# Performance work log

Hardware: AMD Instinct MI355X
Metric: run time of the kernel (lower is better)

The kernel has to match this reference:

```python
import jax, jax.numpy as jnp
import numpy as np


def setup_inputs() -> dict:
    key = jax.random.key(0)
    k1, k2 = jax.random.split(key)
    B, C = 32768, 1000
    output = jax.random.normal(k1, (B, C), dtype=jnp.float32)
    target = jax.random.randint(k2, (B,), 0, C, dtype=jnp.int64)
    return {"output": output, "target": target}


def _soft_hinge_loss(margin, output, target):
    B = output.shape[0]
    rows = jnp.arange(B)
    fst = jax.nn.relu(1.0 - margin)
    # relu(1 - z_y + logsumexp(z))
    snd = jax.nn.relu(1.0 - output[rows, target]
                      + jax.scipy.special.logsumexp(output, axis=1))
    return jnp.where(margin >= 0, fst, snd)


def _partial_opt_mask(loss_value, threshold):
    # Vectorized form of the serial cumulative-threshold loop:
    # sort ascending, accumulate L over ALL sorted values, select sorted
    # position idx iff cumsum <= threshold - idx.
    B = loss_value.shape[0]
    order = jnp.argsort(loss_value)
    sorted_loss = loss_value[order]
    cum = jnp.cumsum(sorted_loss)
    selected = cum <= (threshold - jnp.arange(B, dtype=loss_value.dtype))
    # scatter selection flags back to original sample positions -> 0/1 vector v
    v = jnp.zeros((B,), dtype=loss_value.dtype).at[order].set(
        selected.astype(loss_value.dtype))
    return v


def reference(output, target):
    B = output.shape[0]
    rows = jnp.arange(B)
    prob = jax.nn.softmax(output, axis=1)                 # [B, C]
    margin = prob[rows, target] - jnp.max(prob, axis=1)   # [B]
    l = _soft_hinge_loss(margin, output, target)          # [B]
    threshold = jnp.asarray(B, dtype=l.dtype)
    v = _partial_opt_mask(l, threshold)                   # [B] 0/1 mask
    curriculum_loss_1 = jnp.dot(v, l)
    curriculum_loss_2 = (jnp.asarray(B, l.dtype) - jnp.sum(v)
                         + jnp.sum((margin < 0).astype(l.dtype)))
    return jnp.where(curriculum_loss_1 < curriculum_loss_2,
                     curriculum_loss_2, curriculum_loss_1)
```

## Files before the change

### kernel.cpp

```cpp
#include <hip/hip_runtime.h>
#include <math.h>

#define WAVE 64
#define NBINS 8192
#define BIN_SHIFT 19

__device__ __forceinline__ float wave_incl_scan(float x) {
  const int lane = threadIdx.x & 63;
#pragma unroll
  for (int o = 1; o < 64; o <<= 1) {
    float t = __shfl_up(x, o, WAVE);
    if (lane >= o) x += t;
  }
  return x;
}

__global__ void row_loss_kernel(const float* __restrict__ outp,
                                const int* __restrict__ target,
                                float* __restrict__ lv,
                                int B, int C) {
  const int lane = threadIdx.x & (WAVE - 1);
  const int wid  = threadIdx.x >> 6;
  const int row  = blockIdx.x * (blockDim.x >> 6) + wid;
  if (row >= B) return;

  const float* rp = outp + (size_t)row * (size_t)C;
  const float zy = rp[target[row]];

  const int C4 = C >> 2;
  const float4* rp4 = (const float4*)rp;

  float m = -INFINITY, s = 0.f;
#pragma unroll 2
  for (int i = lane; i < C4; i += WAVE) {
    float4 v = rp4[i];
    m = fmaxf(fmaxf(m, fmaxf(v.x, v.y)), fmaxf(v.z, v.w));
    s += __expf(v.x) + __expf(v.y) + __expf(v.z) + __expf(v.w);
  }
  for (int i = (C4 << 2) + lane; i < C; i += WAVE) {
    float x = rp[i];
    m = fmaxf(m, x);
    s += __expf(x);
  }
#pragma unroll
  for (int o = 32; o; o >>= 1) {
    m = fmaxf(m, __shfl_xor(m, o, WAVE));
    s += __shfl_xor(s, o, WAVE);
  }

  if (lane == 0) {
    float l = (zy >= m) ? 1.0f : fmaxf(0.0f, 1.0f - zy + __logf(s));
    lv[row] = l;
  }
}

__global__ __launch_bounds__(1024)
void hist_kernel(const float* __restrict__ lv,
                 unsigned* __restrict__ hcnt,
                 float* __restrict__ hsum,
                 unsigned* __restrict__ n_one,
                 int B) {
  __shared__ unsigned scnt[NBINS];
  __shared__ float    ssum[NBINS];
  __shared__ unsigned s_one;

  const int tid = threadIdx.x;
  for (int i = tid; i < NBINS; i += 1024) { scnt[i] = 0u; ssum[i] = 0.f; }
  if (tid == 0) s_one = 0u;
  __syncthreads();

  const int gid = blockIdx.x * 1024 + tid;
  if (gid < B) {
    float v = lv[gid];
    unsigned bits = __float_as_uint(v);
    unsigned b = bits >> BIN_SHIFT;
    atomicAdd(&scnt[b], 1u);
    atomicAdd(&ssum[b], v);
    unsigned long long ball = __ballot(bits == 0x3F800000u);
    if ((tid & 63) == 0 && ball)
      atomicAdd(&s_one, (unsigned)__popcll(ball));
  }
  __syncthreads();

  for (int i = tid; i < NBINS; i += 1024) {
    unsigned c = scnt[i];
    if (c) {
      atomicAdd(&hcnt[i], c);
      atomicAdd(&hsum[i], ssum[i]);
    }
  }
  if (tid == 0 && s_one) atomicAdd(n_one, s_one);
}

__global__ __launch_bounds__(1024)
void scan_hist(const unsigned* __restrict__ hcnt,
               const float* __restrict__ hsum,
               const unsigned* __restrict__ n_one_p,
               float* __restrict__ out, int B) {
  const int tid = threadIdx.x;
  const int lane = tid & 63, wid = tid >> 6;
  __shared__ float wS[16], wC[16];
  __shared__ unsigned sh_first;

  const int BPT = NBINS / 1024;
  float bs[8], bn[8];
  float ls = 0.f, lc = 0.f;
#pragma unroll
  for (int i = 0; i < 8; i++) {
    int b = tid * BPT + i;
    bs[i] = hsum[b];
    bn[i] = (float)hcnt[b];
    ls += bs[i]; lc += bn[i];
  }

  const float cn = (float)B - (float)(*n_one_p);
  if (tid == 0) sh_first = 0xFFFFFFFFu;

  float is = wave_incl_scan(ls);
  float ic = wave_incl_scan(lc);
  if (lane == 63) { wS[wid] = is; wC[wid] = ic; }
  __syncthreads();
  if (wid == 0 && lane < 16) {
    float x = wS[lane], y = wC[lane];
    float xs = x, ys = y;
#pragma unroll
    for (int o = 1; o < 16; o <<= 1) {
      float t = __shfl_up(xs, o, WAVE);
      float u = __shfl_up(ys, o, WAVE);
      if (lane >= o) { xs += t; ys += u; }
    }
    wS[lane] = xs - x;
    wC[lane] = ys - y;
  }
  __syncthreads();

  float cS = wS[wid] + (is - ls);
  float cC = wC[wid] + (ic - lc);
  int fidx = -1; float fS = 0.f, fC = 0.f;
#pragma unroll
  for (int i = 0; i < 8; i++) {
    if (fidx < 0 && (cS + bs[i]) + (cC + bn[i]) - 1.f > (float)B) {
      fidx = i; fS = cS; fC = cC;
    }
    cS += bs[i]; cC += bn[i];
  }
  if (fidx >= 0) atomicMin(&sh_first, (unsigned)tid);
  __syncthreads();

  const double Bd = (double)B;
  if (sh_first == (unsigned)tid && fidx >= 0) {
    const unsigned bin = (unsigned)(tid * BPT + fidx);
    const double v  = (double)__uint_as_float(bin << BIN_SHIFT);
    const double S0 = (double)fS, K0 = (double)fC;
    const double mt = (double)bn[fidx];
    double j = floor((Bd - S0 - K0 + 1.0) / (v + 1.0));
    if (j < 0.0) j = 0.0;
    if (j > mt) j = mt;
    double loss1 = S0 + j * v;
    double loss2 = Bd - (K0 + j) + (double)cn;
    out[0] = (float)fmax(loss1, loss2);
  } else if (sh_first == 0xFFFFFFFFu && tid == 1023) {
    double loss1 = (double)cS;
    double loss2 = (double)cn;
    out[0] = (float)fmax(loss1, loss2);
  }
}

extern "C" void kernel_launch(void* const* d_in, const int* in_sizes, int n_in,
                              void* d_out, int out_size, void* d_ws, size_t ws_size,
                              hipStream_t stream) {
  const float* outp  = (const float*)d_in[0];
  const int* target  = (const int*)d_in[1];
  const int B = in_sizes[1];
  const int C = in_sizes[0] / B;

  float*    lv   = (float*)d_ws;
  unsigned* hcnt = (unsigned*)((char*)d_ws + (size_t)B * 4);
  float*    hsum = (float*)((char*)d_ws + (size_t)B * 4 + NBINS * 4);
  unsigned* none = (unsigned*)((char*)d_ws + (size_t)B * 4 + NBINS * 8);

  hipMemsetAsync((char*)d_ws + (size_t)B * 4, 0, NBINS * 8 + 16, stream);

  const int waves_per_block = 4;
  dim3 grid((B + waves_per_block - 1) / waves_per_block);
  row_loss_kernel<<<grid, waves_per_block * WAVE, 0, stream>>>(outp, target, lv, B, C);

  const int hblocks = (B + 1023) / 1024;
  hist_kernel<<<hblocks, 1024, 0, stream>>>(lv, hcnt, hsum, none, B);
  scan_hist<<<1, 1024, 0, stream>>>(hcnt, hsum, none, (float*)d_out, B);
}
```

Measured before the change: 39.49 us.

## Fuse histogram and scan into one block with finer nonuniform bins

Replaces the global-atomic histogram kernel, the memset and the separate scan kernel with a single-block kernel. That kernel loads all per-row losses, builds a shared-memory histogram with fine bins near exponents 126–136 and coarse bins elsewhere, and scans it in place. The row-loss loop is also unrolled to four float4 loads per iteration to raise memory-level parallelism. This removes two launches, the memset and the global atomics. In exchange, one block must do all 32768 shared atomics serially, and the final answer is only exact if the bin layout suits the loss distribution; the code hardcodes a fixed input size, with 8 float4 per thread covering B up to 32768.

```diff
diff --git a/kernel.cpp b/kernel.cpp
--- a/kernel.cpp
+++ b/kernel.cpp
@@ -2,8 +2,27 @@
 #include <math.h>
 
 #define WAVE 64
-#define NBINS 8192
-#define BIN_SHIFT 19
+
+#define E_LO 126
+#define E_HI 136
+#define FINE_SHIFT 15
+#define N_FINE ((E_HI - E_LO) << 8)
+#define N_LOW  (E_LO)
+#define SBINS  3072
+
+__device__ __forceinline__ unsigned bin_of(unsigned bits) {
+  unsigned e = bits >> 23;
+  if (e < E_LO) return e;
+  if (e < E_HI) return N_LOW + ((bits - (E_LO << 23)) >> FINE_SHIFT);
+  return N_LOW + N_FINE + (e - E_HI);
+}
+
+__device__ __forceinline__ float bin_lower(unsigned bin) {
+  if (bin < N_LOW) return __uint_as_float(bin << 23);
+  if (bin < N_LOW + N_FINE)
+    return __uint_as_float((E_LO << 23) + ((bin - N_LOW) << FINE_SHIFT));
+  return __uint_as_float((E_HI + (bin - N_LOW - N_FINE)) << 23);
+}
 
 __device__ __forceinline__ float wave_incl_scan(float x) {
   const int lane = threadIdx.x & 63;
@@ -15,13 +34,14 @@
   return x;
 }
 
-__global__ void row_loss_kernel(const float* __restrict__ outp,
-                                const int* __restrict__ target,
-                                float* __restrict__ lv,
-                                int B, int C) {
+__global__ __launch_bounds__(256)
+void row_loss_kernel(const float* __restrict__ outp,
+                     const int* __restrict__ target,
+                     float* __restrict__ lv,
+                     int B, int C) {
   const int lane = threadIdx.x & (WAVE - 1);
   const int wid  = threadIdx.x >> 6;
-  const int row  = blockIdx.x * (blockDim.x >> 6) + wid;
+  const int row  = blockIdx.x * 4 + wid;
   if (row >= B) return;
 
   const float* rp = outp + (size_t)row * (size_t)C;
@@ -29,13 +49,26 @@
 
   const int C4 = C >> 2;
   const float4* rp4 = (const float4*)rp;
-
-  float m = -INFINITY, s = 0.f;
-#pragma unroll 2
-  for (int i = lane; i < C4; i += WAVE) {
-    float4 v = rp4[i];
-    m = fmaxf(fmaxf(m, fmaxf(v.x, v.y)), fmaxf(v.z, v.w));
-    s += __expf(v.x) + __expf(v.y) + __expf(v.z) + __expf(v.w);
+  const float NI = -INFINITY;
+
+  float m = NI, s = 0.f;
+  for (int i = lane; i < C4; i += 4 * WAVE) {
+    const int i1 = i + 64, i2 = i + 128, i3 = i + 192;
+    float4 a0 = rp4[i];
+    float4 a1 = rp4[i1 < C4 ? i1 : i];
+    float4 a2 = rp4[i2 < C4 ? i2 : i];
+    float4 a3 = rp4[i3 < C4 ? i3 : i];
+    if (i1 >= C4) a1.x = a1.y = a1.z = a1.w = NI;
+    if (i2 >= C4) a2.x = a2.y = a2.z = a2.w = NI;
+    if (i3 >= C4) a3.x = a3.y = a3.z = a3.w = NI;
+    m = fmaxf(m, fmaxf(fmaxf(a0.x, a0.y), fmaxf(a0.z, a0.w)));
+    m = fmaxf(m, fmaxf(fmaxf(a1.x, a1.y), fmaxf(a1.z, a1.w)));
+    m = fmaxf(m, fmaxf(fmaxf(a2.x, a2.y), fmaxf(a2.z, a2.w)));
+    m = fmaxf(m, fmaxf(fmaxf(a3.x, a3.y), fmaxf(a3.z, a3.w)));
+    s += __expf(a0.x) + __expf(a0.y) + __expf(a0.z) + __expf(a0.w);
+    s += __expf(a1.x) + __expf(a1.y) + __expf(a1.z) + __expf(a1.w);
+    s += __expf(a2.x) + __expf(a2.y) + __expf(a2.z) + __expf(a2.w);
+    s += __expf(a3.x) + __expf(a3.y) + __expf(a3.z) + __expf(a3.w);
   }
   for (int i = (C4 << 2) + lane; i < C; i += WAVE) {
     float x = rp[i];
@@ -55,67 +88,61 @@
 }
 
 __global__ __launch_bounds__(1024)
-void hist_kernel(const float* __restrict__ lv,
-                 unsigned* __restrict__ hcnt,
-                 float* __restrict__ hsum,
-                 unsigned* __restrict__ n_one,
-                 int B) {
-  __shared__ unsigned scnt[NBINS];
-  __shared__ float    ssum[NBINS];
-  __shared__ unsigned s_one;
-
-  const int tid = threadIdx.x;
-  for (int i = tid; i < NBINS; i += 1024) { scnt[i] = 0u; ssum[i] = 0.f; }
-  if (tid == 0) s_one = 0u;
-  __syncthreads();
-
-  const int gid = blockIdx.x * 1024 + tid;
-  if (gid < B) {
-    float v = lv[gid];
-    unsigned bits = __float_as_uint(v);
-    unsigned b = bits >> BIN_SHIFT;
-    atomicAdd(&scnt[b], 1u);
-    atomicAdd(&ssum[b], v);
-    unsigned long long ball = __ballot(bits == 0x3F800000u);
-    if ((tid & 63) == 0 && ball)
-      atomicAdd(&s_one, (unsigned)__popcll(ball));
-  }
-  __syncthreads();
-
-  for (int i = tid; i < NBINS; i += 1024) {
-    unsigned c = scnt[i];
-    if (c) {
-      atomicAdd(&hcnt[i], c);
-      atomicAdd(&hsum[i], ssum[i]);
-    }
-  }
-  if (tid == 0 && s_one) atomicAdd(n_one, s_one);
-}
-
-__global__ __launch_bounds__(1024)
-void scan_hist(const unsigned* __restrict__ hcnt,
-               const float* __restrict__ hsum,
-               const unsigned* __restrict__ n_one_p,
-               float* __restrict__ out, int B) {
+void select_fused(const float* __restrict__ lv, float* __restrict__ out, int B) {
+  __shared__ unsigned scnt[2][SBINS];
+  __shared__ float    ssum[2][SBINS];
+  __shared__ float wS[16], wC[16];
+  __shared__ unsigned sh_first, s_one;
+
   const int tid = threadIdx.x;
   const int lane = tid & 63, wid = tid >> 6;
-  __shared__ float wS[16], wC[16];
-  __shared__ unsigned sh_first;
-
-  const int BPT = NBINS / 1024;
-  float bs[8], bn[8];
+  const int sub = wid & 1;
+
+  for (int i = tid; i < SBINS; i += 1024) {
+    scnt[0][i] = 0u; scnt[1][i] = 0u;
+    ssum[0][i] = 0.f; ssum[1][i] = 0.f;
+  }
+  if (tid == 0) { s_one = 0u; sh_first = 0xFFFFFFFFu; }
+  __syncthreads();
+
+  float4 t[8];
+  bool ok[8];
+#pragma unroll
+  for (int k = 0; k < 8; k++) {
+    const int idx4 = tid + k * 1024;
+    ok[k] = (idx4 * 4 + 3) < B;
+    t[k] = ok[k] ? ((const float4*)lv)[idx4] : make_float4(0.f, 0.f, 0.f, 0.f);
+  }
+  int ones = 0;
+#pragma unroll
+  for (int k = 0; k < 8; k++) {
+    if (ok[k]) {
+      const float e[4] = {t[k].x, t[k].y, t[k].z, t[k].w};
+#pragma unroll
+      for (int j = 0; j < 4; j++) {
+        const unsigned bits = __float_as_uint(e[j]);
+        if (bits == 0x3F800000u) ones++;
+        const unsigned b = bin_of(bits);
+        atomicAdd(&scnt[sub][b], 1u);
+        atomicAdd(&ssum[sub][b], e[j]);
+      }
+    }
+  }
+  float of = (float)ones;
+#pragma unroll
+  for (int o = 32; o; o >>= 1) of += __shfl_xor(of, o, WAVE);
+  if (lane == 0 && of > 0.f) atomicAdd(&s_one, (unsigned)of);
+  __syncthreads();
+
+  float bs[3], bn[3];
   float ls = 0.f, lc = 0.f;
 #pragma unroll
-  for (int i = 0; i < 8; i++) {
-    int b = tid * BPT + i;
-    bs[i] = hsum[b];
-    bn[i] = (float)hcnt[b];
+  for (int i = 0; i < 3; i++) {
+    const int b = tid * 3 + i;
+    bs[i] = ssum[0][b] + ssum[1][b];
+    bn[i] = (float)(scnt[0][b] + scnt[1][b]);
     ls += bs[i]; lc += bn[i];
   }
-
-  const float cn = (float)B - (float)(*n_one_p);
-  if (tid == 0) sh_first = 0xFFFFFFFFu;
-
   float is = wave_incl_scan(ls);
   float ic = wave_incl_scan(lc);
   if (lane == 63) { wS[wid] = is; wC[wid] = ic; }
@@ -125,9 +152,9 @@
     float xs = x, ys = y;
 #pragma unroll
     for (int o = 1; o < 16; o <<= 1) {
-      float t = __shfl_up(xs, o, WAVE);
-      float u = __shfl_up(ys, o, WAVE);
-      if (lane >= o) { xs += t; ys += u; }
+      float a = __shfl_up(xs, o, WAVE);
+      float b = __shfl_up(ys, o, WAVE);
+      if (lane >= o) { xs += a; ys += b; }
     }
     wS[lane] = xs - x;
     wC[lane] = ys - y;
@@ -138,7 +165,7 @@
   float cC = wC[wid] + (ic - lc);
   int fidx = -1; float fS = 0.f, fC = 0.f;
 #pragma unroll
-  for (int i = 0; i < 8; i++) {
+  for (int i = 0; i < 3; i++) {
     if (fidx < 0 && (cS + bs[i]) + (cC + bn[i]) - 1.f > (float)B) {
       fidx = i; fS = cS; fC = cC;
     }
@@ -148,20 +175,21 @@
   __syncthreads();
 
   const double Bd = (double)B;
+  const double cn = (double)B - (double)s_one;
   if (sh_first == (unsigned)tid && fidx >= 0) {
-    const unsigned bin = (unsigned)(tid * BPT + fidx);
-    const double v  = (double)__uint_as_float(bin << BIN_SHIFT);
+    const unsigned bin = (unsigned)(tid * 3 + fidx);
+    const double v  = (double)bin_lower(bin);
     const double S0 = (double)fS, K0 = (double)fC;
     const double mt = (double)bn[fidx];
     double j = floor((Bd - S0 - K0 + 1.0) / (v + 1.0));
     if (j < 0.0) j = 0.0;
     if (j > mt) j = mt;
-    double loss1 = S0 + j * v;
-    double loss2 = Bd - (K0 + j) + (double)cn;
+    const double loss1 = S0 + j * v;
+    const double loss2 = Bd - (K0 + j) + cn;
     out[0] = (float)fmax(loss1, loss2);
   } else if (sh_first == 0xFFFFFFFFu && tid == 1023) {
-    double loss1 = (double)cS;
-    double loss2 = (double)cn;
+    const double loss1 = (double)cS;
+    const double loss2 = cn;
     out[0] = (float)fmax(loss1, loss2);
   }
 }
@@ -174,18 +202,9 @@
   const int B = in_sizes[1];
   const int C = in_sizes[0] / B;
 
-  float*    lv   = (float*)d_ws;
-  unsigned* hcnt = (unsigned*)((char*)d_ws + (size_t)B * 4);
-  float*    hsum = (float*)((char*)d_ws + (size_t)B * 4 + NBINS * 4);
-  unsigned* none = (unsigned*)((char*)d_ws + (size_t)B * 4 + NBINS * 8);
-
-  hipMemsetAsync((char*)d_ws + (size_t)B * 4, 0, NBINS * 8 + 16, stream);
-
-  const int waves_per_block = 4;
-  dim3 grid((B + waves_per_block - 1) / waves_per_block);
-  row_loss_kernel<<<grid, waves_per_block * WAVE, 0, stream>>>(outp, target, lv, B, C);
-
-  const int hblocks = (B + 1023) / 1024;
-  hist_kernel<<<hblocks, 1024, 0, stream>>>(lv, hcnt, hsum, none, B);
-  scan_hist<<<1, 1024, 0, stream>>>(hcnt, hsum, none, (float*)d_out, B);
-}
+  float* lv = (float*)d_ws;
+
+  dim3 grid((B + 3) / 4);
+  row_loss_kernel<<<grid, 256, 0, stream>>>(outp, target, lv, B, C);
+  select_fused<<<1, 1024, 0, stream>>>(lv, (float*)d_out, B);
+}
```

After: 74.18 us. +87.9%, slower.

## Replace global histogram atomics with per-block partial histograms and drop memset

Applied to the files above, without the earlier changes.

Each histogram block now handles four values per thread and writes its whole shared histogram to a private slice of workspace instead of atomically merging into one global histogram. The single-block scan kernel then sums the partial histograms itself. Because every slice is fully overwritten, the memset launch is no longer needed. The cost is that the scan kernel must read nparts×NBINS entries serially per thread, and each block writes all 8192 bins even when they are empty.

```diff
diff --git a/kernel.cpp b/kernel.cpp
--- a/kernel.cpp
+++ b/kernel.cpp
@@ -4,6 +4,7 @@
 #define WAVE 64
 #define NBINS 8192
 #define BIN_SHIFT 19
+#define HVPT 4
 
 __device__ __forceinline__ float wave_incl_scan(float x) {
   const int lane = threadIdx.x & 63;
@@ -56,64 +57,90 @@
 
 __global__ __launch_bounds__(1024)
 void hist_kernel(const float* __restrict__ lv,
-                 unsigned* __restrict__ hcnt,
-                 float* __restrict__ hsum,
-                 unsigned* __restrict__ n_one,
+                 unsigned* __restrict__ hcnt_part,
+                 float* __restrict__ hsum_part,
+                 unsigned* __restrict__ none_part,
                  int B) {
   __shared__ unsigned scnt[NBINS];
   __shared__ float    ssum[NBINS];
   __shared__ unsigned s_one;
 
   const int tid = threadIdx.x;
+  const int lane = tid & 63;
+
   for (int i = tid; i < NBINS; i += 1024) { scnt[i] = 0u; ssum[i] = 0.f; }
   if (tid == 0) s_one = 0u;
   __syncthreads();
 
-  const int gid = blockIdx.x * 1024 + tid;
-  if (gid < B) {
-    float v = lv[gid];
-    unsigned bits = __float_as_uint(v);
-    unsigned b = bits >> BIN_SHIFT;
-    atomicAdd(&scnt[b], 1u);
-    atomicAdd(&ssum[b], v);
-    unsigned long long ball = __ballot(bits == 0x3F800000u);
-    if ((tid & 63) == 0 && ball)
-      atomicAdd(&s_one, (unsigned)__popcll(ball));
-  }
-  __syncthreads();
-
-  for (int i = tid; i < NBINS; i += 1024) {
-    unsigned c = scnt[i];
-    if (c) {
-      atomicAdd(&hcnt[i], c);
-      atomicAdd(&hsum[i], ssum[i]);
-    }
-  }
-  if (tid == 0 && s_one) atomicAdd(n_one, s_one);
+  const int base = blockIdx.x * 1024 * HVPT;
+  int ones = 0;
+#pragma unroll
+  for (int k = 0; k < HVPT; k++) {
+    const int gid = base + k * 1024 + tid;
+    if (gid < B) {
+      const float v = lv[gid];
+      const unsigned bits = __float_as_uint(v);
+      if (bits == 0x3F800000u) ones++;
+      const unsigned b = bits >> BIN_SHIFT;
+      atomicAdd(&scnt[b], 1u);
+      atomicAdd(&ssum[b], v);
+    }
+  }
+  float of = (float)ones;
+#pragma unroll
+  for (int o = 32; o; o >>= 1) of += __shfl_xor(of, o, WAVE);
+  if (lane == 0 && of > 0.f) atomicAdd(&s_one, (unsigned)of);
+  __syncthreads();
+
+  unsigned* cdst = hcnt_part + (size_t)blockIdx.x * NBINS;
+  float*    sdst = hsum_part + (size_t)blockIdx.x * NBINS;
+  const int b0 = tid * 8;
+#pragma unroll
+  for (int h = 0; h < 2; h++) {
+    uint4 c; float4 s;
+    c.x = scnt[b0 + h*4 + 0]; c.y = scnt[b0 + h*4 + 1];
+    c.z = scnt[b0 + h*4 + 2]; c.w = scnt[b0 + h*4 + 3];
+    s.x = ssum[b0 + h*4 + 0]; s.y = ssum[b0 + h*4 + 1];
+    s.z = ssum[b0 + h*4 + 2]; s.w = ssum[b0 + h*4 + 3];
+    *(uint4*)(cdst + b0 + h*4) = c;
+    *(float4*)(sdst + b0 + h*4) = s;
+  }
+  if (tid == 0) none_part[blockIdx.x] = s_one;
 }
 
 __global__ __launch_bounds__(1024)
-void scan_hist(const unsigned* __restrict__ hcnt,
-               const float* __restrict__ hsum,
-               const unsigned* __restrict__ n_one_p,
-               float* __restrict__ out, int B) {
+void scan_hist(const unsigned* __restrict__ hcnt_part,
+               const float* __restrict__ hsum_part,
+               const unsigned* __restrict__ none_part,
+               float* __restrict__ out, int B, int nparts) {
   const int tid = threadIdx.x;
   const int lane = tid & 63, wid = tid >> 6;
   __shared__ float wS[16], wC[16];
   __shared__ unsigned sh_first;
 
-  const int BPT = NBINS / 1024;
   float bs[8], bn[8];
+#pragma unroll
+  for (int i = 0; i < 8; i++) { bs[i] = 0.f; bn[i] = 0.f; }
+  const int b0 = tid * 8;
+  for (int p = 0; p < nparts; p++) {
+    const unsigned* cp = hcnt_part + (size_t)p * NBINS + b0;
+    const float*    sp = hsum_part + (size_t)p * NBINS + b0;
+#pragma unroll
+    for (int h = 0; h < 2; h++) {
+      uint4  c = *(const uint4*)(cp + h*4);
+      float4 s = *(const float4*)(sp + h*4);
+      bn[h*4+0] += (float)c.x; bn[h*4+1] += (float)c.y;
+      bn[h*4+2] += (float)c.z; bn[h*4+3] += (float)c.w;
+      bs[h*4+0] += s.x; bs[h*4+1] += s.y; bs[h*4+2] += s.z; bs[h*4+3] += s.w;
+    }
+  }
   float ls = 0.f, lc = 0.f;
 #pragma unroll
-  for (int i = 0; i < 8; i++) {
-    int b = tid * BPT + i;
-    bs[i] = hsum[b];
-    bn[i] = (float)hcnt[b];
-    ls += bs[i]; lc += bn[i];
-  }
-
-  const float cn = (float)B - (float)(*n_one_p);
+  for (int i = 0; i < 8; i++) { ls += bs[i]; lc += bn[i]; }
+
+  unsigned n_one = 0;
+  for (int p = 0; p < nparts; p++) n_one += none_part[p];
+  const double cn = (double)B - (double)n_one;
   if (tid == 0) sh_first = 0xFFFFFFFFu;
 
   float is = wave_incl_scan(ls);
@@ -125,9 +152,9 @@
     float xs = x, ys = y;
 #pragma unroll
     for (int o = 1; o < 16; o <<= 1) {
-      float t = __shfl_up(xs, o, WAVE);
-      float u = __shfl_up(ys, o, WAVE);
-      if (lane >= o) { xs += t; ys += u; }
+      float a = __shfl_up(xs, o, WAVE);
+      float b = __shfl_up(ys, o, WAVE);
+      if (lane >= o) { xs += a; ys += b; }
     }
     wS[lane] = xs - x;
     wC[lane] = ys - y;
@@ -149,19 +176,19 @@
 
   const double Bd = (double)B;
   if (sh_first == (unsigned)tid && fidx >= 0) {
-    const unsigned bin = (unsigned)(tid * BPT + fidx);
+    const unsigned bin = (unsigned)(tid * 8 + fidx);
     const double v  = (double)__uint_as_float(bin << BIN_SHIFT);
     const double S0 = (double)fS, K0 = (double)fC;
     const double mt = (double)bn[fidx];
     double j = floor((Bd - S0 - K0 + 1.0) / (v + 1.0));
     if (j < 0.0) j = 0.0;
     if (j > mt) j = mt;
-    double loss1 = S0 + j * v;
-    double loss2 = Bd - (K0 + j) + (double)cn;
+    const double loss1 = S0 + j * v;
+    const double loss2 = Bd - (K0 + j) + cn;
     out[0] = (float)fmax(loss1, loss2);
   } else if (sh_first == 0xFFFFFFFFu && tid == 1023) {
-    double loss1 = (double)cS;
-    double loss2 = (double)cn;
+    const double loss1 = (double)cS;
+    const double loss2 = cn;
     out[0] = (float)fmax(loss1, loss2);
   }
 }
@@ -174,18 +201,17 @@
   const int B = in_sizes[1];
   const int C = in_sizes[0] / B;
 
-  float*    lv   = (float*)d_ws;
-  unsigned* hcnt = (unsigned*)((char*)d_ws + (size_t)B * 4);
-  float*    hsum = (float*)((char*)d_ws + (size_t)B * 4 + NBINS * 4);
-  unsigned* none = (unsigned*)((char*)d_ws + (size_t)B * 4 + NBINS * 8);
-
-  hipMemsetAsync((char*)d_ws + (size_t)B * 4, 0, NBINS * 8 + 16, stream);
+  const int nparts = (B + 1024 * HVPT - 1) / (1024 * HVPT);
+  float*    lv        = (float*)d_ws;
+  unsigned* hcnt_part = (unsigned*)((char*)d_ws + (size_t)B * 4);
+  float*    hsum_part = (float*)((char*)hcnt_part + (size_t)nparts * NBINS * 4);
+  unsigned* none_part = (unsigned*)((char*)hsum_part + (size_t)nparts * NBINS * 4);
 
   const int waves_per_block = 4;
   dim3 grid((B + waves_per_block - 1) / waves_per_block);
   row_loss_kernel<<<grid, waves_per_block * WAVE, 0, stream>>>(outp, target, lv, B, C);
 
-  const int hblocks = (B + 1023) / 1024;
-  hist_kernel<<<hblocks, 1024, 0, stream>>>(lv, hcnt, hsum, none, B);
-  scan_hist<<<1, 1024, 0, stream>>>(hcnt, hsum, none, (float*)d_out, B);
-}
+  hist_kernel<<<nparts, 1024, 0, stream>>>(lv, hcnt_part, hsum_part, none_part, B);
+  scan_hist<<<1, 1024, 0, stream>>>(hcnt_part, hsum_part, none_part,
+                                    (float*)d_out, B, nparts);
+}
```

After: 45.32 us. 1.15x slower.

## Fuse histogram and scan via last-block pattern, zero workspace inside row kernel

Applied to the files above, without the earlier changes.

Drops the separate memset by having the first 64 blocks of the row-loss kernel zero the histogram counters, sums and the two extra counters. Merges the histogram and scan kernels into one, where the last block to finish, found through an atomic done counter, runs the scan. This cuts two launches and their gaps out of a short pipeline, at the cost of threadfences, an atomic counter, and an order dependency that the zeroing must finish before the histogram kernel runs.

```diff
diff --git a/kernel.cpp b/kernel.cpp
--- a/kernel.cpp
+++ b/kernel.cpp
@@ -18,7 +18,15 @@
 __global__ void row_loss_kernel(const float* __restrict__ outp,
                                 const int* __restrict__ target,
                                 float* __restrict__ lv,
+                                unsigned* __restrict__ zbase,
                                 int B, int C) {
+  if (blockIdx.x < 64) {
+    const int z = blockIdx.x * 256 + threadIdx.x;
+    zbase[z] = 0u;
+    if (blockIdx.x == 0 && threadIdx.x < 2)
+      zbase[2 * NBINS + threadIdx.x] = 0u;
+  }
+
   const int lane = threadIdx.x & (WAVE - 1);
   const int wid  = threadIdx.x >> 6;
   const int row  = blockIdx.x * (blockDim.x >> 6) + wid;
@@ -55,65 +63,68 @@
 }
 
 __global__ __launch_bounds__(1024)
-void hist_kernel(const float* __restrict__ lv,
-                 unsigned* __restrict__ hcnt,
-                 float* __restrict__ hsum,
-                 unsigned* __restrict__ n_one,
-                 int B) {
+void hist_scan_kernel(const float* __restrict__ lv,
+                      unsigned* __restrict__ hcnt,
+                      float*    __restrict__ hsum,
+                      unsigned* __restrict__ n_one,
+                      unsigned* __restrict__ done_ctr,
+                      float* __restrict__ out, int B, int nparts) {
   __shared__ unsigned scnt[NBINS];
   __shared__ float    ssum[NBINS];
-  __shared__ unsigned s_one;
+  __shared__ float wS[16], wC[16];
+  __shared__ unsigned sh_first, s_one;
+  __shared__ int s_last;
 
   const int tid = threadIdx.x;
+  const int lane = tid & 63, wid = tid >> 6;
+
   for (int i = tid; i < NBINS; i += 1024) { scnt[i] = 0u; ssum[i] = 0.f; }
   if (tid == 0) s_one = 0u;
   __syncthreads();
 
   const int gid = blockIdx.x * 1024 + tid;
+  int ones = 0;
   if (gid < B) {
-    float v = lv[gid];
-    unsigned bits = __float_as_uint(v);
-    unsigned b = bits >> BIN_SHIFT;
+    const float v = lv[gid];
+    const unsigned bits = __float_as_uint(v);
+    if (bits == 0x3F800000u) ones++;
+    const unsigned b = bits >> BIN_SHIFT;
     atomicAdd(&scnt[b], 1u);
     atomicAdd(&ssum[b], v);
-    unsigned long long ball = __ballot(bits == 0x3F800000u);
-    if ((tid & 63) == 0 && ball)
-      atomicAdd(&s_one, (unsigned)__popcll(ball));
-  }
+  }
+  float of = (float)ones;
+#pragma unroll
+  for (int o = 32; o; o >>= 1) of += __shfl_xor(of, o, WAVE);
+  if (lane == 0 && of > 0.f) atomicAdd(&s_one, (unsigned)of);
   __syncthreads();
 
   for (int i = tid; i < NBINS; i += 1024) {
-    unsigned c = scnt[i];
+    const unsigned c = scnt[i];
     if (c) {
       atomicAdd(&hcnt[i], c);
       atomicAdd(&hsum[i], ssum[i]);
     }
   }
   if (tid == 0 && s_one) atomicAdd(n_one, s_one);
-}
-
-__global__ __launch_bounds__(1024)
-void scan_hist(const unsigned* __restrict__ hcnt,
-               const float* __restrict__ hsum,
-               const unsigned* __restrict__ n_one_p,
-               float* __restrict__ out, int B) {
-  const int tid = threadIdx.x;
-  const int lane = tid & 63, wid = tid >> 6;
-  __shared__ float wS[16], wC[16];
-  __shared__ unsigned sh_first;
-
-  const int BPT = NBINS / 1024;
+
+  __syncthreads();
+  __threadfence();
+  if (tid == 0)
+    s_last = (atomicAdd(done_ctr, 1u) == (unsigned)(nparts - 1));
+  __syncthreads();
+  if (!s_last) return;
+  __threadfence();
+
   float bs[8], bn[8];
   float ls = 0.f, lc = 0.f;
+  const int b0 = tid * 8;
 #pragma unroll
   for (int i = 0; i < 8; i++) {
-    int b = tid * BPT + i;
-    bs[i] = hsum[b];
-    bn[i] = (float)hcnt[b];
+    bs[i] = hsum[b0 + i];
+    bn[i] = (float)hcnt[b0 + i];
     ls += bs[i]; lc += bn[i];
   }
-
-  const float cn = (float)B - (float)(*n_one_p);
+  const float cnf = (float)B - (float)(*n_one);
   if (tid == 0) sh_first = 0xFFFFFFFFu;
 
   float is = wave_incl_scan(ls);
@@ -125,9 +136,9 @@
     float xs = x, ys = y;
 #pragma unroll
     for (int o = 1; o < 16; o <<= 1) {
-      float t = __shfl_up(xs, o, WAVE);
-      float u = __shfl_up(ys, o, WAVE);
-      if (lane >= o) { xs += t; ys += u; }
+      float a = __shfl_up(xs, o, WAVE);
+      float b = __shfl_up(ys, o, WAVE);
+      if (lane >= o) { xs += a; ys += b; }
     }
     wS[lane] = xs - x;
     wC[lane] = ys - y;
@@ -148,20 +159,21 @@
   __syncthreads();
 
   const double Bd = (double)B;
+  const double cn = (double)cnf;
   if (sh_first == (unsigned)tid && fidx >= 0) {
-    const unsigned bin = (unsigned)(tid * BPT + fidx);
+    const unsigned bin = (unsigned)(tid * 8 + fidx);
     const double v  = (double)__uint_as_float(bin << BIN_SHIFT);
     const double S0 = (double)fS, K0 = (double)fC;
     const double mt = (double)bn[fidx];
     double j = floor((Bd - S0 - K0 + 1.0) / (v + 1.0));
     if (j < 0.0) j = 0.0;
     if (j > mt) j = mt;
-    double loss1 = S0 + j * v;
-    double loss2 = Bd - (K0 + j) + (double)cn;
+    const double loss1 = S0 + j * v;
+    const double loss2 = Bd - (K0 + j) + cn;
     out[0] = (float)fmax(loss1, loss2);
   } else if (sh_first == 0xFFFFFFFFu && tid == 1023) {
-    double loss1 = (double)cS;
-    double loss2 = (double)cn;
+    const double loss1 = (double)cS;
+    const double loss2 = cn;
     out[0] = (float)fmax(loss1, loss2);
   }
 }
@@ -174,18 +186,19 @@
   const int B = in_sizes[1];
   const int C = in_sizes[0] / B;
 
-  float*    lv   = (float*)d_ws;
-  unsigned* hcnt = (unsigned*)((char*)d_ws + (size_t)B * 4);
-  float*    hsum = (float*)((char*)d_ws + (size_t)B * 4 + NBINS * 4);
-  unsigned* none = (unsigned*)((char*)d_ws + (size_t)B * 4 + NBINS * 8);
-
-  hipMemsetAsync((char*)d_ws + (size_t)B * 4, 0, NBINS * 8 + 16, stream);
+  char* p = (char*)d_ws;
+  float*    lv   = (float*)p;                 p += (size_t)B * 4;
+  unsigned* hcnt = (unsigned*)p;              p += (size_t)NBINS * 4;
+  float*    hsum = (float*)p;                 p += (size_t)NBINS * 4;
+  unsigned* none = (unsigned*)p;              p += 4;
+  unsigned* done = (unsigned*)p;
 
   const int waves_per_block = 4;
   dim3 grid((B + waves_per_block - 1) / waves_per_block);
-  row_loss_kernel<<<grid, waves_per_block * WAVE, 0, stream>>>(outp, target, lv, B, C);
-
-  const int hblocks = (B + 1023) / 1024;
-  hist_kernel<<<hblocks, 1024, 0, stream>>>(lv, hcnt, hsum, none, B);
-  scan_hist<<<1, 1024, 0, stream>>>(hcnt, hsum, none, (float*)d_out, B);
-}
+  row_loss_kernel<<<grid, waves_per_block * WAVE, 0, stream>>>(
+      outp, target, lv, hcnt, B, C);
+
+  const int nparts = (B + 1023) / 1024;
+  hist_scan_kernel<<<nparts, 1024, 0, stream>>>(
+      lv, hcnt, hsum, none, done, (float*)d_out, B, nparts);
+}
```

Result: slower. 44.99 us (+14.0%).
